# Kernel optimization log

Measured on AMD Instinct MI355X. Metric: run time of the kernel, lower is better.

The kernel has to match this reference:

```python
import jax, jax.numpy as jnp
import numpy as np
import math

B, S, D, H, DFF = 4, 1024, 1024, 16, 4096
DH = D // H
ALPHA = 1.0
NEG = -1e20
EPS = 1e-5


def layernorm(x, g, b):
    mu = jnp.mean(x, axis=-1, keepdims=True)
    var = jnp.mean((x - mu) ** 2, axis=-1, keepdims=True)
    return (x - mu) * jax.lax.rsqrt(var + EPS) * g + b


def setup_inputs() -> dict:
    key = jax.random.key(0)
    ks = jax.random.split(key, 16)
    sc = 1.0 / math.sqrt(D)
    inp = {
        "x": jax.random.normal(ks[0], (B, S, D), jnp.float32),
        "mask": jnp.ones((B, 1, S), jnp.float32),
        "Wq": jax.random.normal(ks[1], (D, D), jnp.float32) * sc,
        "Wk": jax.random.normal(ks[2], (D, D), jnp.float32) * sc,
        "Wv": jax.random.normal(ks[3], (D, D), jnp.float32) * sc,
        "ln1_g": jnp.ones((DH,), jnp.float32),
        "ln1_b": jnp.zeros((DH,), jnp.float32),
        "Wo": jax.random.normal(ks[4], (D, D), jnp.float32) * sc,
        "bo": jnp.zeros((D,), jnp.float32),
        "ln2_g": jnp.ones((D,), jnp.float32),
        "ln2_b": jnp.zeros((D,), jnp.float32),
        "Ws": jax.random.normal(ks[5], (D, D), jnp.float32) * sc,
        "Wh": jax.random.normal(ks[6], (D, D), jnp.float32) * sc,
        "b_f": jnp.zeros((D,), jnp.float32),
        "lnfg_g": jnp.ones((D,), jnp.float32),
        "lnfg_b": jnp.zeros((D,), jnp.float32),
        "Wp1": jax.random.normal(ks[7], (DFF, D), jnp.float32) * sc,
        "bp1": jnp.zeros((DFF,), jnp.float32),
        "Wp2": jax.random.normal(ks[8], (D, DFF), jnp.float32) / math.sqrt(DFF),
        "bp2": jnp.zeros((D,), jnp.float32),
        "lnffn_g": jnp.ones((D,), jnp.float32),
        "lnffn_b": jnp.zeros((D,), jnp.float32),
    }
    return inp


def reference(x, mask, Wq, Wk, Wv, ln1_g, ln1_b, Wo, bo, ln2_g, ln2_b,
              Ws, Wh, b_f, lnfg_g, lnfg_b, Wp1, bp1, Wp2, bp2, lnffn_g, lnffn_b):
    b, s, d = x.shape
    # --- masked multi-head attention ---
    q = (x @ Wq.T).reshape(b, s, H, DH)
    k = (x @ Wk.T).reshape(b, s, H, DH)
    v = (x @ Wv.T).reshape(b, s, H, DH)
    q = layernorm(q, ln1_g, ln1_b)
    k = layernorm(k, ln1_g, ln1_b)
    v = layernorm(v, ln1_g, ln1_b)
    energy = jnp.einsum('nqhd,nkhd->nhqk', q, k)  # (B,H,S,S)
    # directional mask: forward pass -> strictly lower triangular allowed (0), else -1e20
    idx = jnp.arange(s)
    allowed = idx[:, None] > idx[None, :]  # tril(diagonal=-1)
    dir_mask = jnp.where(allowed, 0.0, NEG).astype(x.dtype)  # (S,S)
    m = jnp.broadcast_to(mask, (b, H, s))  # (B,H,S)
    pair = m[:, :, :, None] * m[:, :, None, :]  # (B,H,S,S)
    final_mask = pair * dir_mask[None, None]
    dist_mask = -jnp.abs(idx[:, None] - idx[None, :]).astype(x.dtype)  # (S,S)
    pre = energy / math.sqrt(d) + final_mask + ALPHA * dist_mask[None, None]
    attn = jax.nn.softmax(pre, axis=-1)
    # faithful to source einsum 'nhql,nlhd->nlhd' (sums attention over q)
    out = jnp.einsum('nhql,nlhd->nlhd', attn, v)
    out = out.reshape(b, s, d)
    out = out @ Wo.T + bo
    h = layernorm(out, ln2_g, ln2_b)
    # --- fusion gate and norm ---
    s_f = layernorm(x @ Ws.T, lnfg_g, lnfg_b)
    h_f = layernorm(h @ Wh.T, lnfg_g, lnfg_b)
    f = jax.nn.sigmoid(s_f + h_f + b_f)
    g = layernorm(f * s_f + (1.0 - f) * h_f, lnfg_g, lnfg_b)
    # --- position-wise FFN + residual + norm ---
    ff = jax.nn.relu(g @ Wp1.T + bp1) @ Wp2.T + bp2
    return layernorm(ff + g, lnffn_g, lnffn_b)
```

## Files before the change

kernel.cpp:

```cpp
#include <hip/hip_runtime.h>

constexpr int CB   = 4;
constexpr int CS   = 1024;
constexpr int CD   = 1024;
constexpr int CH   = 16;
constexpr int CDFF = 4096;
constexpr int CNT  = CB * CS;

typedef unsigned short ush;
typedef __bf16 bf16_t;
typedef bf16_t bf16x8 __attribute__((ext_vector_type(8)));
typedef float  f32x4  __attribute__((ext_vector_type(4)));

__device__ __forceinline__ ush f2bf(float f) {
    union { float f; unsigned u; } v; v.f = f;
    unsigned u = v.u;
    return (ush)((u + 0x7fffu + ((u >> 16) & 1u)) >> 16);
}
__device__ __forceinline__ float bf2f(ush h) {
    union { unsigned u; float f; } v; v.u = ((unsigned)h) << 16;
    return v.f;
}

__device__ __forceinline__ void gll16(const void* g, void* l) {
    __builtin_amdgcn_global_load_lds((const __attribute__((address_space(1))) void*)g,
                                     (__attribute__((address_space(3))) void*)l,
                                     16, 0, 0);
}

constexpr int Q4 = (CD * CD) / 4;
__global__ __launch_bounds__(256) void k_convert_all(
        const float4* __restrict__ Wq, const float4* __restrict__ Wk,
        const float4* __restrict__ Wv, const float4* __restrict__ Ws,
        const float4* __restrict__ Wo, const float4* __restrict__ Wh,
        const float4* __restrict__ Wp1, const float4* __restrict__ Wp2,
        const float4* __restrict__ x, ushort4* __restrict__ arena,
        ushort4* __restrict__ xb) {
    int i = blockIdx.x * 256 + threadIdx.x;
    int stride = gridDim.x * 256;
    for (; i < 18 * Q4; i += stride) {
        const float4* src; int off; ushort4* dst;
        if (i < 4 * Q4) {
            if (i < 2 * Q4) { if (i < Q4)     { src = Wq; off = i; }          else { src = Wk; off = i - Q4; } }
            else            { if (i < 3 * Q4) { src = Wv; off = i - 2 * Q4; } else { src = Ws; off = i - 3 * Q4; } }
            dst = arena + i;
        } else if (i < 6 * Q4) {
            if (i < 5 * Q4) { src = Wo; off = i - 4 * Q4; } else { src = Wh; off = i - 5 * Q4; }
            dst = arena + i;
        } else if (i < 14 * Q4) {
            if (i < 10 * Q4) { src = Wp1; off = i - 6 * Q4; } else { src = Wp2; off = i - 10 * Q4; }
            dst = arena + i;
        } else {
            src = x; off = i - 14 * Q4; dst = xb + off;
        }
        float4 v = src[off];
        ushort4 o;
        o.x = f2bf(v.x); o.y = f2bf(v.y); o.z = f2bf(v.z); o.w = f2bf(v.w);
        *dst = o;
    }
}

__global__ __launch_bounds__(256) void k_zero(float* __restrict__ p, int n) {
    int i = blockIdx.x * 256 + threadIdx.x;
    int stride = gridDim.x * 256;
    for (; i < n; i += stride) p[i] = 0.f;
}

template <int TN, int EPI, int SPLITK>
__global__ __launch_bounds__(256, 4) void k_gemm_bt(
        const ush* __restrict__ A, const ush* __restrict__ Bm,
        float* __restrict__ C, ush* __restrict__ Cb,
        const float* __restrict__ bias, const float* __restrict__ bias2,
        ush* __restrict__ out2, ush* __restrict__ out3,
        int N, int K) {
    constexpr int NJ  = TN / 32;
    constexpr int BCH = TN / 32;
    __shared__ ush As[128 * 64];
    __shared__ ush Bs[TN * 64];
    const int tid  = threadIdx.x;
    const int wave = tid >> 6, lane = tid & 63;
    const int quad = lane >> 4, r = lane & 15;
    const int wm = wave >> 1, wn = wave & 1;
    const int bm = blockIdx.x, bn = blockIdx.y;

    const int kcnt  = K / SPLITK;
    const int kbase = blockIdx.z * kcnt;
    if (SPLITK > 1) C += (size_t)blockIdx.z * (size_t)gridDim.x * 128 * N;

    const int trow = tid >> 3, tk8 = tid & 7;
    const int kcl  = tk8 ^ (trow & 7);
    const ush* ap = A  + (size_t)(bm * 128 + trow) * K + kbase + kcl * 8;
    const ush* bp = Bm + (size_t)(bn * TN  + trow) * K + kbase + kcl * 8;
    ush* asd = As + tid * 8;
    ush* bsd = Bs + tid * 8;
    const size_t cstep = (size_t)32 * K;

    f32x4 acc[4][NJ];
#pragma unroll
    for (int i = 0; i < 4; i++)
#pragma unroll
        for (int j = 0; j < NJ; j++) acc[i][j] = (f32x4){0.f, 0.f, 0.f, 0.f};

    const int rx = r & 7;
    for (int k0 = 0; k0 < kcnt; k0 += 64) {
#pragma unroll
        for (int c = 0; c < 4; c++)   gll16(ap + c * cstep, asd + c * 2048);
#pragma unroll
        for (int c = 0; c < BCH; c++) gll16(bp + c * cstep, bsd + c * 2048);
        ap += 64; bp += 64;
        __syncthreads();
#pragma unroll
        for (int h = 0; h < 2; h++) {
            const int kx = (((h << 2) | quad) ^ rx) * 8;
            bf16x8 af[4], bfv[NJ];
#pragma unroll
            for (int i = 0; i < 4; i++)
                af[i] = *(const bf16x8*)(As + (wm * 64 + i * 16 + r) * 64 + kx);
#pragma unroll
            for (int j = 0; j < NJ; j++)
                bfv[j] = *(const bf16x8*)(Bs + (wn * (TN / 2) + j * 16 + r) * 64 + kx);
#pragma unroll
            for (int i = 0; i < 4; i++)
#pragma unroll
                for (int j = 0; j < NJ; j++)
                    acc[i][j] = __builtin_amdgcn_mfma_f32_16x16x32_bf16(af[i], bfv[j], acc[i][j], 0, 0, 0);
        }
        __syncthreads();
    }

    if (EPI == 4) {
        if (bn >= 24) {
            const int colb = (bn - 24) * 128 + wn * 64;
#pragma unroll
            for (int i = 0; i < 4; i++) {
                const int row0 = bm * 128 + wm * 64 + i * 16 + quad * 4;
#pragma unroll
                for (int j = 0; j < NJ; j++) {
                    const int col = colb + j * 16 + r;
#pragma unroll
                    for (int g = 0; g < 4; g++)
                        C[(size_t)(row0 + g) * 1024 + col] = acc[i][j][g];
                }
            }
        } else {
            float g4[4], b4[4];
#pragma unroll
            for (int j = 0; j < 4; j++) { g4[j] = bias[j * 16 + r]; b4[j] = bias2[j * 16 + r]; }
            ush* dst; int cb0 = bn * 128 + wn * 64;
            if (bn < 8)       dst = Cb;
            else if (bn < 16) { dst = out2; cb0 -= 1024; }
            else              { dst = out3; cb0 -= 2048; }
#pragma unroll
            for (int i = 0; i < 4; i++) {
                const int row0 = bm * 128 + wm * 64 + i * 16 + quad * 4;
#pragma unroll
                for (int g = 0; g < 4; g++) {
                    float s = 0.f, q = 0.f;
#pragma unroll
                    for (int j = 0; j < 4; j++) { float v = acc[i][j][g]; s += v; q += v * v; }
                    s += __shfl_xor(s, 1); q += __shfl_xor(q, 1);
                    s += __shfl_xor(s, 2); q += __shfl_xor(q, 2);
                    s += __shfl_xor(s, 4); q += __shfl_xor(q, 4);
                    s += __shfl_xor(s, 8); q += __shfl_xor(q, 8);
                    float mu   = s * (1.f / 64.f);
                    float rstd = rsqrtf(q * (1.f / 64.f) - mu * mu + 1e-5f);
#pragma unroll
                    for (int j = 0; j < 4; j++) {
                        float y = (acc[i][j][g] - mu) * rstd * g4[j] + b4[j];
                        dst[(size_t)(row0 + g) * 1024 + cb0 + j * 16 + r] = f2bf(y);
                    }
                }
            }
        }
    } else {
#pragma unroll
        for (int i = 0; i < 4; i++) {
            const int row0 = bm * 128 + wm * 64 + i * 16 + quad * 4;
#pragma unroll
            for (int j = 0; j < NJ; j++) {
                const int col = bn * TN + wn * (TN / 2) + j * 16 + r;
                float bv = (EPI == 3) ? bias[col] : 0.f;
#pragma unroll
                for (int g = 0; g < 4; g++) {
                    float v = acc[i][j][g] + bv;
                    size_t off = (size_t)(row0 + g) * N + col;
                    if (EPI == 3) { v = fmaxf(v, 0.f); Cb[off] = f2bf(v); }
                    else          { C[off] = v; }
                }
            }
        }
    }
}

__global__ __launch_bounds__(256) void k_attn(const ush* __restrict__ qb,
                                              const ush* __restrict__ kb,
                                              const float* __restrict__ mask,
                                              float* __restrict__ wcol) {
    __shared__ ush   Qs[64][72];
    __shared__ ush   Ks[64][72];
    __shared__ float colpart[4][64];

    const int tid  = threadIdx.x;
    const int wave = tid >> 6, lane = tid & 63;
    const int quad = lane >> 4, r = lane & 15;
    const int bh = blockIdx.x, bi = bh >> 4, hi = bh & 15;
    const int q0 = blockIdx.y * 64;

    {
        int row = tid >> 2, seg = (tid & 3) * 16;
        const ush* src = qb + ((size_t)(bi * CS + q0 + row) * CD + hi * 64 + seg);
        *(uint4*)&Qs[row][seg]     = *(const uint4*)src;
        *(uint4*)&Qs[row][seg + 8] = *(const uint4*)(src + 8);
    }
    __syncthreads();
    bf16x8 af0 = *(const bf16x8*)&Qs[wave * 16 + r][quad * 8];
    bf16x8 af1 = *(const bf16x8*)&Qs[wave * 16 + r][32 + quad * 8];

    float mq[4];
#pragma unroll
    for (int g = 0; g < 4; g++) mq[g] = mask[bi * CS + q0 + wave * 16 + quad * 4 + g];

    const int t0 = (q0 >= 128) ? 0 : ((q0 >= 64) ? 1 : 2);
    float pr[3][4][4];
    float s_loc[4] = {0.f, 0.f, 0.f, 0.f};

    for (int t = t0; t < 3; t++) {
        const int l0 = q0 - 128 + t * 64;
        __syncthreads();
        {
            int row = tid >> 2, seg = (tid & 3) * 16;
            const ush* src = kb + ((size_t)(bi * CS + l0 + row) * CD + hi * 64 + seg);
            *(uint4*)&Ks[row][seg]     = *(const uint4*)src;
            *(uint4*)&Ks[row][seg + 8] = *(const uint4*)(src + 8);
        }
        __syncthreads();
#pragma unroll
        for (int jt = 0; jt < 4; jt++) {
            bf16x8 bf0 = *(const bf16x8*)&Ks[jt * 16 + r][quad * 8];
            bf16x8 bf1 = *(const bf16x8*)&Ks[jt * 16 + r][32 + quad * 8];
            f32x4 sc = (f32x4){0.f, 0.f, 0.f, 0.f};
            sc = __builtin_amdgcn_mfma_f32_16x16x32_bf16(af0, bf0, sc, 0, 0, 0);
            sc = __builtin_amdgcn_mfma_f32_16x16x32_bf16(af1, bf1, sc, 0, 0, 0);
            const int l = l0 + jt * 16 + r;
            const float ml = mask[bi * CS + l];
#pragma unroll
            for (int g = 0; g < 4; g++) {
                const int qg = q0 + wave * 16 + quad * 4 + g;
                float e  = sc[g] * 0.03125f;
                float mv = (qg > l) ? 0.f : mq[g] * ml * (-1e20f);
                float p  = __expf(e + mv - fabsf((float)(qg - l)) - 8.f);
                pr[t][jt][g] = p;
                s_loc[g] += p;
            }
        }
    }

    float rs[4];
#pragma unroll
    for (int g = 0; g < 4; g++) {
        float s = s_loc[g];
        s += __shfl_xor(s, 1); s += __shfl_xor(s, 2);
        s += __shfl_xor(s, 4); s += __shfl_xor(s, 8);
        rs[g] = (s > 0.f) ? 1.f / s : 0.f;
    }

    for (int t = t0; t < 3; t++) {
        const int l0 = q0 - 128 + t * 64;
#pragma unroll
        for (int jt = 0; jt < 4; jt++) {
            float csum = 0.f;
#pragma unroll
            for (int g = 0; g < 4; g++) csum += pr[t][jt][g] * rs[g];
            csum += __shfl_xor(csum, 16);
            csum += __shfl_xor(csum, 32);
            if (quad == 0) colpart[wave][jt * 16 + r] = csum;
        }
        __syncthreads();
        if (tid < 64) {
            float v = colpart[0][tid] + colpart[1][tid] + colpart[2][tid] + colpart[3][tid];
            atomicAdd(&wcol[(size_t)bh * CS + l0 + tid], v);
        }
        __syncthreads();
    }
}

__global__ __launch_bounds__(256) void k_scale_v(const ush* __restrict__ vb,
                                                 const float* __restrict__ wcol,
                                                 ush* __restrict__ out) {
    int i = blockIdx.x * 256 + threadIdx.x;
    int stride = gridDim.x * 256;
    for (; i < CNT * CD; i += stride) {
        int token = i >> 10;
        int c = i & (CD - 1);
        int l = token & (CS - 1);
        int b = token >> 10;
        int h = c >> 6;
        float w = wcol[(size_t)(b * CH + h) * CS + l] + (1.f / 1024.f);
        out[i] = f2bf(w * bf2f(vb[i]));
    }
}

__device__ __forceinline__ void blk_stats(float s, float q, float* red,
                                          int wave, int lane, float& mu, float& rstd) {
#pragma unroll
    for (int off = 32; off >= 1; off >>= 1) {
        s += __shfl_xor(s, off);
        q += __shfl_xor(q, off);
    }
    if (lane == 0) { red[wave] = s; red[4 + wave] = q; }
    __syncthreads();
    s = red[0] + red[1] + red[2] + red[3];
    q = red[4] + red[5] + red[6] + red[7];
    mu = s * (1.f / 1024.f);
    rstd = rsqrtf(q * (1.f / 1024.f) - mu * mu + 1e-5f);
    __syncthreads();
}

template <int MODE>
__global__ __launch_bounds__(256) void k_ln_row(const float* __restrict__ in0,
                                                const float* __restrict__ in1,
                                                const float* __restrict__ in2,
                                                const float* __restrict__ badd,
                                                const float* __restrict__ gam,
                                                const float* __restrict__ bet,
                                                float* __restrict__ outf,
                                                ush* __restrict__ outb) {
    __shared__ float red[8];
    const int tid = threadIdx.x, wave = tid >> 6, lane = tid & 63;
    const size_t base = (size_t)blockIdx.x * CD;
    float t[4], sf[4];
#pragma unroll
    for (int j = 0; j < 4; j++) {
        int col = tid + j * 256;
        if (MODE == 0)      t[j] = in0[base + col] + in1[base + col] + badd[col];
        else if (MODE == 1) t[j] = in0[base + col];
        else if (MODE == 2) { sf[j] = in0[base + col]; t[j] = in1[base + col] + in2[base + col]; }
        else                t[j] = in0[base + col] + in1[base + col] + in2[base + col] + badd[col];
    }
    float s = 0.f, q = 0.f, mu, rstd;
#pragma unroll
    for (int j = 0; j < 4; j++) { s += t[j]; q += t[j] * t[j]; }
    blk_stats(s, q, red, wave, lane, mu, rstd);

    if (MODE == 2) {
#pragma unroll
        for (int j = 0; j < 4; j++) {
            int col = tid + j * 256;
            float hf = (t[j] - mu) * rstd * gam[col] + bet[col];
            float f  = 1.f / (1.f + __expf(-(sf[j] + hf + badd[col])));
            t[j] = f * sf[j] + (1.f - f) * hf;
        }
        s = 0.f; q = 0.f;
#pragma unroll
        for (int j = 0; j < 4; j++) { s += t[j]; q += t[j] * t[j]; }
        blk_stats(s, q, red, wave, lane, mu, rstd);
    }

#pragma unroll
    for (int j = 0; j < 4; j++) {
        int col = tid + j * 256;
        float y = (t[j] - mu) * rstd * gam[col] + bet[col];
        if (MODE == 0)      outb[base + col] = f2bf(y);
        else if (MODE == 1) outf[base + col] = y;
        else if (MODE == 2) { outf[base + col] = y; outb[base + col] = f2bf(y); }
        else                outf[base + col] = y;
    }
}

extern "C" void kernel_launch(void* const* d_in, const int* in_sizes, int n_in,
                              void* d_out, int out_size, void* d_ws, size_t ws_size,
                              hipStream_t stream) {
    const float* x    = (const float*)d_in[0];
    const float* mask = (const float*)d_in[1];
    const float* Wq   = (const float*)d_in[2];
    const float* Wk   = (const float*)d_in[3];
    const float* Wv   = (const float*)d_in[4];
    const float* ln1g = (const float*)d_in[5];
    const float* ln1b = (const float*)d_in[6];
    const float* Wo   = (const float*)d_in[7];
    const float* bo   = (const float*)d_in[8];
    const float* ln2g = (const float*)d_in[9];
    const float* ln2b = (const float*)d_in[10];
    const float* Ws   = (const float*)d_in[11];
    const float* Wh   = (const float*)d_in[12];
    const float* bf_  = (const float*)d_in[13];
    const float* lnfgg = (const float*)d_in[14];
    const float* lnfgb = (const float*)d_in[15];
    const float* Wp1  = (const float*)d_in[16];
    const float* bp1  = (const float*)d_in[17];
    const float* Wp2  = (const float*)d_in[18];
    const float* bp2  = (const float*)d_in[19];
    const float* lnffg = (const float*)d_in[20];
    const float* lnffb = (const float*)d_in[21];
    float* out = (float*)d_out;

    char* p = (char*)d_ws;
    auto alloc = [&](size_t bytes) -> char* {
        char* r = p;
        p += (bytes + 255) & ~(size_t)255;
        return r;
    };
    ush*   arena = (ush*)alloc((size_t)14 * CD * CD * 2);
    ush*   Wob   = arena + (size_t)4 * CD * CD;
    ush*   Whb   = arena + (size_t)5 * CD * CD;
    ush*   Wp1b  = arena + (size_t)6 * CD * CD;
    ush*   Wp2b  = arena + (size_t)10 * CD * CD;
    ush*   xb    = (ush*)alloc((size_t)CNT * CD * 2);
    ush*   klnb  = (ush*)alloc((size_t)CNT * CD * 2);
    ush*   vb    = (ush*)alloc((size_t)CNT * CD * 2);
    ush*   qlnb  = (ush*)alloc((size_t)CNT * CD * 2);
    ush*   gb    = (ush*)alloc((size_t)CNT * CD * 2);
    float* P0    = (float*)alloc((size_t)2 * CNT * CD * 4);
    float* P1    = P0 + (size_t)CNT * CD;
    ush*   ff1b  = (ush*)alloc((size_t)CNT * CDFF * 2);
    float* bufS  = (float*)alloc((size_t)CNT * CD * 4);
    float* wcol  = (float*)alloc((size_t)CB * CH * CS * 4);
    float* sbuf  = (float*)ff1b;
    ush*   attb  = qlnb;
    ush*   hb    = klnb;
    float* bufG  = (float*)vb;

    dim3 blk(256);

    k_convert_all<<<dim3(8192), blk, 0, stream>>>(
        (const float4*)Wq, (const float4*)Wk, (const float4*)Wv, (const float4*)Ws,
        (const float4*)Wo, (const float4*)Wh, (const float4*)Wp1, (const float4*)Wp2,
        (const float4*)x, (ushort4*)arena, (ushort4*)xb);

    k_gemm_bt<128, 4, 1><<<dim3(32, 32, 1), blk, 0, stream>>>(
        xb, arena, sbuf, qlnb, ln1g, ln1b, klnb, vb, 4096, CD);

    k_ln_row<1><<<dim3(CNT), blk, 0, stream>>>(sbuf, nullptr, nullptr, nullptr,
                                               lnfgg, lnfgb, bufS, nullptr);

    k_zero<<<dim3(64), blk, 0, stream>>>(wcol, CB * CH * CS);
    k_attn<<<dim3(CB * CH, CS / 64), blk, 0, stream>>>(qlnb, klnb, mask, wcol);
    k_scale_v<<<dim3(4096), blk, 0, stream>>>(vb, wcol, attb);

    k_gemm_bt<64, 0, 2><<<dim3(32, 16, 2), blk, 0, stream>>>(
        attb, Wob, P0, nullptr, nullptr, nullptr, nullptr, nullptr, CD, CD);
    k_ln_row<0><<<dim3(CNT), blk, 0, stream>>>(P0, P1, nullptr, bo, ln2g, ln2b, nullptr, hb);

    k_gemm_bt<64, 0, 2><<<dim3(32, 16, 2), blk, 0, stream>>>(
        hb, Whb, P0, nullptr, nullptr, nullptr, nullptr, nullptr, CD, CD);
    k_ln_row<2><<<dim3(CNT), blk, 0, stream>>>(bufS, P0, P1, bf_, lnfgg, lnfgb, bufG, gb);

    k_gemm_bt<128, 3, 1><<<dim3(32, 32, 1), blk, 0, stream>>>(
        gb, Wp1b, nullptr, ff1b, bp1, nullptr, nullptr, nullptr, CDFF, CD);
    k_gemm_bt<64, 0, 2><<<dim3(32, 16, 2), blk, 0, stream>>>(
        ff1b, Wp2b, P0, nullptr, nullptr, nullptr, nullptr, nullptr, CD, CDFF);
    k_ln_row<3><<<dim3(CNT), blk, 0, stream>>>(P0, P1, bufG, bp2, lnffg, lnffb, out, nullptr);

    (void)in_sizes; (void)n_in; (void)out_size; (void)ws_size;
}
```

Baseline: 381.0 us.

## Store GEMM intermediates in bf16 and fold LN/zero kernels into neighbours

Split-K partials, the Ws projection output, and the gate output g are now written and read as bf16 instead of fp32. This halves intermediate memory traffic. The standalone LN pass over x@Ws is removed by recomputing that layernorm inside the fusion-gate kernel, and zeroing of wcol moves into the conversion kernel, which drops two launches. The cost is lower precision, because split-K partial sums and the residual input g are rounded to bf16 before they are summed.

New measurement: 362.1 us. 1.05x faster.

```diff
diff --git a/kernel.cpp b/kernel.cpp
--- a/kernel.cpp
+++ b/kernel.cpp
@@ -35,9 +35,11 @@
         const float4* __restrict__ Wo, const float4* __restrict__ Wh,
         const float4* __restrict__ Wp1, const float4* __restrict__ Wp2,
         const float4* __restrict__ x, ushort4* __restrict__ arena,
-        ushort4* __restrict__ xb) {
+        ushort4* __restrict__ xb, float4* __restrict__ wz) {
     int i = blockIdx.x * 256 + threadIdx.x;
     int stride = gridDim.x * 256;
+    for (int i2 = i; i2 < (CB * CH * CS) / 4; i2 += stride)
+        wz[i2] = (float4){0.f, 0.f, 0.f, 0.f};
     for (; i < 18 * Q4; i += stride) {
         const float4* src; int off; ushort4* dst;
         if (i < 4 * Q4) {
@@ -60,18 +62,12 @@
     }
 }
 
-__global__ __launch_bounds__(256) void k_zero(float* __restrict__ p, int n) {
-    int i = blockIdx.x * 256 + threadIdx.x;
-    int stride = gridDim.x * 256;
-    for (; i < n; i += stride) p[i] = 0.f;
-}
-
 template <int TN, int EPI, int SPLITK>
 __global__ __launch_bounds__(256, 4) void k_gemm_bt(
         const ush* __restrict__ A, const ush* __restrict__ Bm,
-        float* __restrict__ C, ush* __restrict__ Cb,
+        ush* __restrict__ Cb,
         const float* __restrict__ bias, const float* __restrict__ bias2,
-        ush* __restrict__ out2, ush* __restrict__ out3,
+        ush* __restrict__ out2, ush* __restrict__ out3, ush* __restrict__ sb,
         int N, int K) {
     constexpr int NJ  = TN / 32;
     constexpr int BCH = TN / 32;
@@ -85,7 +81,8 @@
 
     const int kcnt  = K / SPLITK;
     const int kbase = blockIdx.z * kcnt;
-    if (SPLITK > 1) C += (size_t)blockIdx.z * (size_t)gridDim.x * 128 * N;
+    ush* dst0 = Cb;
+    if (SPLITK > 1) dst0 += (size_t)blockIdx.z * (size_t)gridDim.x * 128 * N;
 
     const int trow = tid >> 3, tk8 = tid & 7;
     const int kcl  = tk8 ^ (trow & 7);
@@ -139,7 +136,7 @@
                     const int col = colb + j * 16 + r;
 #pragma unroll
                     for (int g = 0; g < 4; g++)
-                        C[(size_t)(row0 + g) * 1024 + col] = acc[i][j][g];
+                        sb[(size_t)(row0 + g) * 1024 + col] = f2bf(acc[i][j][g]);
                 }
             }
         } else {
@@ -184,8 +181,8 @@
                 for (int g = 0; g < 4; g++) {
                     float v = acc[i][j][g] + bv;
                     size_t off = (size_t)(row0 + g) * N + col;
-                    if (EPI == 3) { v = fmaxf(v, 0.f); Cb[off] = f2bf(v); }
-                    else          { C[off] = v; }
+                    if (EPI == 3) v = fmaxf(v, 0.f);
+                    dst0[off] = f2bf(v);
                 }
             }
         }
@@ -317,9 +314,9 @@
 }
 
 template <int MODE>
-__global__ __launch_bounds__(256) void k_ln_row(const float* __restrict__ in0,
-                                                const float* __restrict__ in1,
-                                                const float* __restrict__ in2,
+__global__ __launch_bounds__(256) void k_ln_row(const ush* __restrict__ b0,
+                                                const ush* __restrict__ b1,
+                                                const ush* __restrict__ b2,
                                                 const float* __restrict__ badd,
                                                 const float* __restrict__ gam,
                                                 const float* __restrict__ bet,
@@ -328,42 +325,55 @@
     __shared__ float red[8];
     const int tid = threadIdx.x, wave = tid >> 6, lane = tid & 63;
     const size_t base = (size_t)blockIdx.x * CD;
-    float t[4], sf[4];
-#pragma unroll
-    for (int j = 0; j < 4; j++) {
-        int col = tid + j * 256;
-        if (MODE == 0)      t[j] = in0[base + col] + in1[base + col] + badd[col];
-        else if (MODE == 1) t[j] = in0[base + col];
-        else if (MODE == 2) { sf[j] = in0[base + col]; t[j] = in1[base + col] + in2[base + col]; }
-        else                t[j] = in0[base + col] + in1[base + col] + in2[base + col] + badd[col];
-    }
+    float t[4], sr[4];
     float s = 0.f, q = 0.f, mu, rstd;
-#pragma unroll
-    for (int j = 0; j < 4; j++) { s += t[j]; q += t[j] * t[j]; }
-    blk_stats(s, q, red, wave, lane, mu, rstd);
 
     if (MODE == 2) {
+#pragma unroll
+        for (int j = 0; j < 4; j++) {
+            int col = tid + j * 256;
+            sr[j] = bf2f(b0[base + col]);
+            t[j]  = bf2f(b1[base + col]) + bf2f(b2[base + col]);
+        }
+#pragma unroll
+        for (int j = 0; j < 4; j++) { s += sr[j]; q += sr[j] * sr[j]; }
+        blk_stats(s, q, red, wave, lane, mu, rstd);
+#pragma unroll
+        for (int j = 0; j < 4; j++) {
+            int col = tid + j * 256;
+            sr[j] = (sr[j] - mu) * rstd * gam[col] + bet[col];
+        }
+        s = 0.f; q = 0.f;
+#pragma unroll
+        for (int j = 0; j < 4; j++) { s += t[j]; q += t[j] * t[j]; }
+        blk_stats(s, q, red, wave, lane, mu, rstd);
 #pragma unroll
         for (int j = 0; j < 4; j++) {
             int col = tid + j * 256;
             float hf = (t[j] - mu) * rstd * gam[col] + bet[col];
-            float f  = 1.f / (1.f + __expf(-(sf[j] + hf + badd[col])));
-            t[j] = f * sf[j] + (1.f - f) * hf;
-        }
-        s = 0.f; q = 0.f;
-#pragma unroll
-        for (int j = 0; j < 4; j++) { s += t[j]; q += t[j] * t[j]; }
-        blk_stats(s, q, red, wave, lane, mu, rstd);
-    }
+            float f  = 1.f / (1.f + __expf(-(sr[j] + hf + badd[col])));
+            t[j] = f * sr[j] + (1.f - f) * hf;
+        }
+    } else {
+#pragma unroll
+        for (int j = 0; j < 4; j++) {
+            int col = tid + j * 256;
+            if (MODE == 0) t[j] = bf2f(b0[base + col]) + bf2f(b1[base + col]) + badd[col];
+            else           t[j] = bf2f(b0[base + col]) + bf2f(b1[base + col]) + bf2f(b2[base + col]) + badd[col];
+        }
+    }
+
+    s = 0.f; q = 0.f;
+#pragma unroll
+    for (int j = 0; j < 4; j++) { s += t[j]; q += t[j] * t[j]; }
+    blk_stats(s, q, red, wave, lane, mu, rstd);
 
 #pragma unroll
     for (int j = 0; j < 4; j++) {
         int col = tid + j * 256;
         float y = (t[j] - mu) * rstd * gam[col] + bet[col];
-        if (MODE == 0)      outb[base + col] = f2bf(y);
-        else if (MODE == 1) outf[base + col] = y;
-        else if (MODE == 2) { outf[base + col] = y; outb[base + col] = f2bf(y); }
-        else                outf[base + col] = y;
+        if (MODE == 3) outf[base + col] = y;
+        else           outb[base + col] = f2bf(y);
     }
 }
 
@@ -410,46 +420,40 @@
     ush*   vb    = (ush*)alloc((size_t)CNT * CD * 2);
     ush*   qlnb  = (ush*)alloc((size_t)CNT * CD * 2);
     ush*   gb    = (ush*)alloc((size_t)CNT * CD * 2);
-    float* P0    = (float*)alloc((size_t)2 * CNT * CD * 4);
-    float* P1    = P0 + (size_t)CNT * CD;
+    ush*   P     = (ush*)alloc((size_t)2 * CNT * CD * 2);
+    ush*   P1    = P + (size_t)CNT * CD;
     ush*   ff1b  = (ush*)alloc((size_t)CNT * CDFF * 2);
-    float* bufS  = (float*)alloc((size_t)CNT * CD * 4);
     float* wcol  = (float*)alloc((size_t)CB * CH * CS * 4);
-    float* sbuf  = (float*)ff1b;
+    ush*   sbuf  = ff1b;
     ush*   attb  = qlnb;
     ush*   hb    = klnb;
-    float* bufG  = (float*)vb;
 
     dim3 blk(256);
 
     k_convert_all<<<dim3(8192), blk, 0, stream>>>(
         (const float4*)Wq, (const float4*)Wk, (const float4*)Wv, (const float4*)Ws,
         (const float4*)Wo, (const float4*)Wh, (const float4*)Wp1, (const float4*)Wp2,
-        (const float4*)x, (ushort4*)arena, (ushort4*)xb);
+        (const float4*)x, (ushort4*)arena, (ushort4*)xb, (float4*)wcol);
 
     k_gemm_bt<128, 4, 1><<<dim3(32, 32, 1), blk, 0, stream>>>(
-        xb, arena, sbuf, qlnb, ln1g, ln1b, klnb, vb, 4096, CD);
-
-    k_ln_row<1><<<dim3(CNT), blk, 0, stream>>>(sbuf, nullptr, nullptr, nullptr,
-                                               lnfgg, lnfgb, bufS, nullptr);
-
-    k_zero<<<dim3(64), blk, 0, stream>>>(wcol, CB * CH * CS);
+        xb, arena, qlnb, ln1g, ln1b, klnb, vb, sbuf, 4096, CD);
+
     k_attn<<<dim3(CB * CH, CS / 64), blk, 0, stream>>>(qlnb, klnb, mask, wcol);
     k_scale_v<<<dim3(4096), blk, 0, stream>>>(vb, wcol, attb);
 
     k_gemm_bt<64, 0, 2><<<dim3(32, 16, 2), blk, 0, stream>>>(
-        attb, Wob, P0, nullptr, nullptr, nullptr, nullptr, nullptr, CD, CD);
-    k_ln_row<0><<<dim3(CNT), blk, 0, stream>>>(P0, P1, nullptr, bo, ln2g, ln2b, nullptr, hb);
+        attb, Wob, P, nullptr, nullptr, nullptr, nullptr, nullptr, CD, CD);
+    k_ln_row<0><<<dim3(CNT), blk, 0, stream>>>(P, P1, nullptr, bo, ln2g, ln2b, nullptr, hb);
 
     k_gemm_bt<64, 0, 2><<<dim3(32, 16, 2), blk, 0, stream>>>(
-        hb, Whb, P0, nullptr, nullptr, nullptr, nullptr, nullptr, CD, CD);
-    k_ln_row<2><<<dim3(CNT), blk, 0, stream>>>(bufS, P0, P1, bf_, lnfgg, lnfgb, bufG, gb);
+        hb, Whb, P, nullptr, nullptr, nullptr, nullptr, nullptr, CD, CD);
+    k_ln_row<2><<<dim3(CNT), blk, 0, stream>>>(sbuf, P, P1, bf_, lnfgg, lnfgb, nullptr, gb);
 
     k_gemm_bt<128, 3, 1><<<dim3(32, 32, 1), blk, 0, stream>>>(
-        gb, Wp1b, nullptr, ff1b, bp1, nullptr, nullptr, nullptr, CDFF, CD);
+        gb, Wp1b, ff1b, bp1, nullptr, nullptr, nullptr, nullptr, CDFF, CD);
     k_gemm_bt<64, 0, 2><<<dim3(32, 16, 2), blk, 0, stream>>>(
-        ff1b, Wp2b, P0, nullptr, nullptr, nullptr, nullptr, nullptr, CD, CDFF);
-    k_ln_row<3><<<dim3(CNT), blk, 0, stream>>>(P0, P1, bufG, bp2, lnffg, lnffb, out, nullptr);
+        ff1b, Wp2b, P, nullptr, nullptr, nullptr, nullptr, nullptr, CD, CDFF);
+    k_ln_row<3><<<dim3(CNT), blk, 0, stream>>>(P, P1, gb, bp2, lnffg, lnffb, out, nullptr);
 
     (void)in_sizes; (void)n_in; (void)out_size; (void)ws_size;
 }
```
